# Optimization experiments

Hardware: AMD Instinct MI355X
Metric: run time of the kernel (lower is better)

Reference implementation:

```python
import jax, jax.numpy as jnp
import numpy as np

B, H, W = 32, 256, 256
K = 8          # nonzero voting centers per image
NPIX = 6       # corner pixels per center
MARGIN = 10.0
RATIO_INV = 1e4
LW = {'center': 1.0, 'corner': 1.0, 'corner_offset': 0.25, 'corner_bin_offset': 1.0}


def setup_inputs() -> dict:
    rng = np.random.default_rng(0)
    out0 = rng.standard_normal((B, 7, H, W)).astype(np.float32)
    out1 = rng.standard_normal((B, 7, H, W)).astype(np.float32)
    t_corner = np.zeros((B, 1, H, W), np.float32)
    t_corner_offset = np.zeros((B, 1, 2, H, W), np.float32)
    t_bin = rng.uniform(-0.5, 0.5, (B, 1, 2, H, W)).astype(np.float32)
    anchors = np.zeros((B, K + 1), np.int32)
    positives = np.zeros((B, K + 1), np.int32)
    neg_zero = np.zeros((B, K + 1), np.int32)
    neg_other = np.zeros((B, K), np.int32)
    for b in range(B):
        flat = rng.choice(H * W, size=K * NPIX, replace=False)
        ys, xs = flat // W, flat % W
        t_corner[b, 0, ys, xs] = 1.0
        cvals = rng.choice(np.arange(1, 1000), K, replace=False).astype(np.float32)
        for k in range(K):
            s = slice(k * NPIX, (k + 1) * NPIX)
            v = cvals[k] - (ys[s] + xs[s]).astype(np.float32)
            t_corner_offset[b, 0, 0, ys[s], xs[s]] = 0.5 * v
            t_corner_offset[b, 0, 1, ys[s], xs[s]] = 0.5 * v
        # reproduce the source's voting_map and its random triplet mining
        vm = t_corner_offset[b, 0, 0] + t_corner_offset[b, 0, 1]
        cy, cx = np.nonzero(t_corner[b, 0])
        vm = vm.copy()
        vm[cy, cx] += (cy + cx).astype(np.float32)
        vals = np.unique(vm)  # [0, c1..cK] sorted, zero first
        zero_flat = np.flatnonzero(vm.ravel() == 0)
        nz_flat = np.flatnonzero(vm.ravel() != 0)
        for ci, cv in enumerate(vals):
            idx = np.flatnonzero(vm.ravel() == cv)
            if cv == 0:
                a, p = rng.choice(idx, 2, replace=False)
                anchors[b, ci], positives[b, ci] = a, p
                neg_zero[b, ci] = rng.choice(nz_flat)
            else:
                if len(idx) > 1:
                    a, p = rng.choice(idx, 2, replace=False)
                else:
                    a = p = idx[0]
                anchors[b, ci], positives[b, ci] = a, p
                neg_zero[b, ci] = rng.choice(zero_flat)
                other = np.flatnonzero((vm.ravel() != 0) & (vm.ravel() != cv))
                neg_other[b, ci - 1] = rng.choice(other)
    return {
        'out0': jnp.asarray(out0), 'out1': jnp.asarray(out1),
        't_corner': jnp.asarray(t_corner),
        't_corner_offset': jnp.asarray(t_corner_offset),
        't_bin': jnp.asarray(t_bin),
        'anchors': jnp.asarray(anchors), 'positives': jnp.asarray(positives),
        'neg_zero': jnp.asarray(neg_zero), 'neg_other': jnp.asarray(neg_other),
    }


def _smooth_l1(d):
    ad = jnp.abs(d)
    return jnp.where(ad < 1.0, 0.5 * d * d, ad - 0.5)


def _losses_one_stack(output, t_corner, t_corner_offset, t_bin,
                      anchors, positives, neg_zero, neg_other):
    # output: [B,7,H,W] -> channel-major [7,B,H,W] (matches transpose(0,1).reshape)
    o = jnp.transpose(output, (1, 0, 2, 3))
    center = o[0]                                   # [B,H,W]  (n_jtyp=1)
    corner = o[1:3]                                 # [2,B,H,W]
    scale = jnp.array([H, W], jnp.float32)[:, None, None, None]
    corner_offset = jnp.tanh(o[3:5]) * scale        # [2,B,H,W]
    corner_bin = o[5:7]                             # [2,B,H,W]
    pos = t_corner[:, 0]                            # [B,H,W]

    # --- triplet loss on center predictions (pre-mined indices) ---
    pdf = center.reshape(B, -1)                     # [B,HW]
    va = jnp.take_along_axis(pdf, anchors, 1)       # [B,K+1]
    vp = jnp.take_along_axis(pdf, positives, 1)
    vn1 = jnp.take_along_axis(pdf, neg_zero, 1)
    vn2 = jnp.take_along_axis(pdf, neg_other, 1)    # [B,K]
    Dap = (va - vp) ** 2
    h1 = jax.nn.relu(Dap - (va - vn1) ** 2 + MARGIN)
    h2 = jax.nn.relu(Dap[:, 1:] - (va[:, 1:] - vn2) ** 2 + MARGIN)
    per_center = h1.at[:, 1:].set(0.5 * (h1[:, 1:] + h2))  # nonzero centers avg 2 hinges
    l_center = jnp.mean(jnp.sum(per_center, axis=1) / (K + 1))

    # --- corner cross entropy (ratio-weighted) ---
    nlogp = -jax.nn.log_softmax(corner, axis=0)     # [2,B,H,W]
    l_corner = jnp.mean(pos * nlogp[1] * RATIO_INV + (1.0 - pos) * nlogp[0], axis=(1, 2))

    # --- corner offset smooth-L1 heatmap loss, summed over the 2 coords ---
    tgt = jnp.transpose(t_corner_offset[:, 0], (1, 0, 2, 3))  # [2,B,H,W]
    mask = jnp.where(tgt != 0, RATIO_INV, 1.0)
    l_co = jnp.sum(jnp.mean(mask * _smooth_l1(corner_offset - tgt), axis=(2, 3)), axis=0)

    # --- corner bin offset sigmoid L1 with corner mask, summed over 2 coords ---
    tb = jnp.transpose(t_bin[:, 0], (1, 0, 2, 3))   # [2,B,H,W]
    w = jnp.mean(pos, axis=(1, 2), keepdims=True)   # [B,1,1]
    w = jnp.where(w == 0, 1.0, w)
    lb = jnp.abs(jax.nn.sigmoid(corner_bin) - 0.5 - tb) * (pos / w)[None]
    l_bo = jnp.sum(jnp.mean(lb, axis=(2, 3)), axis=0)

    return jnp.concatenate([
        jnp.array([l_center * LW['center']]),
        l_corner * LW['corner'],
        l_co * LW['corner_offset'],
        l_bo * LW['corner_bin_offset'],
    ])  # [1 + 3B]


def reference(out0, out1, t_corner, t_corner_offset, t_bin,
              anchors, positives, neg_zero, neg_other):
    s0 = _losses_one_stack(out0, t_corner, t_corner_offset, t_bin,
                           anchors, positives, neg_zero, neg_other)
    s1 = _losses_one_stack(out1, t_corner, t_corner_offset, t_bin,
                           anchors, positives, neg_zero, neg_other)
    return jnp.stack([s0, s1])  # [2, 1+3B]
```

## Files before the change

### kernel.cpp

```cpp
#include <hip/hip_runtime.h>

#define BB 32
#define HH 256
#define WW 256
#define HW (HH*WW)
#define HW4 (HW/4)
#define KP1 9
#define KNEG 8
#define MARGIN_F 10.0f
#define RATIO_INV_F 10000.0f

#define SLOT(i) ((i)*16)
#define WS_BYTES (226*16*4)

#define NSCAN 512
#define NGATH 4
#define NCE   1024
#define NCO   1024
#define GRID  (NSCAN + NGATH + NCE + NCO)

__device__ __forceinline__ float fast_tanh(float x) {
    float xc = fminf(fmaxf(x, -15.f), 15.f);
    float t = __expf(2.f * xc);
    return (t - 1.f) / (t + 1.f);
}
__device__ __forceinline__ float fast_sigmoid(float x) {
    return 1.f / (1.f + __expf(-x));
}
__device__ __forceinline__ float smooth_l1(float d) {
    float ad = fabsf(d);
    return ad < 1.f ? 0.5f * d * d : ad - 0.5f;
}
__device__ __forceinline__ float el(const float4& v, int j) {
    return reinterpret_cast<const float*>(&v)[j];
}
__device__ __forceinline__ float nlse0(float c0, float c1) {
    const float mx = fmaxf(c0, c1);
    return mx + __logf(1.f + __expf(-fabsf(c0 - c1))) - c0;
}
__device__ __forceinline__ void block_reduce_atomic(float x, float* dst,
                                                    float* scratch) {
    const int lane = threadIdx.x & 63;
    const int wid  = threadIdx.x >> 6;
#pragma unroll
    for (int off = 32; off; off >>= 1) x += __shfl_down(x, off);
    __syncthreads();
    if (lane == 0) scratch[wid] = x;
    __syncthreads();
    if (threadIdx.x == 0)
        atomicAdd(dst, scratch[0] + scratch[1] + scratch[2] + scratch[3]);
}

__global__ __launch_bounds__(256) void ml_fused_kernel(
    const float* __restrict__ out0, const float* __restrict__ out1,
    const float* __restrict__ t_corner, const float* __restrict__ t_co,
    const float* __restrict__ t_bin,
    const int* __restrict__ anchors, const int* __restrict__ positives,
    const int* __restrict__ neg_zero, const int* __restrict__ neg_other,
    float* __restrict__ acc)
{
    __shared__ float scratch[4];
    const int bid = blockIdx.x;
    const int t = threadIdx.x;

    if (bid < NSCAN) {
        const int b = bid >> 4;
        const int base = (bid & 15) * 1024;
        const float4* tc4 = (const float4*)(t_corner + (size_t)b * HW);
        float4 v[4];
#pragma unroll
        for (int k = 0; k < 4; ++k) v[k] = tc4[base + k * 256 + t];
        float s_pos = 0.f;
#pragma unroll
        for (int k = 0; k < 4; ++k) {
#pragma unroll
            for (int j = 0; j < 4; ++j) {
                const float pv = el(v[k], j);
                if (pv != 0.f) {
                    s_pos += pv;
                    const int p = 4 * (base + k * 256 + t) + j;
                    const float* oa = out0 + (size_t)b * 7 * HW;
                    const float* ob = out1 + (size_t)b * 7 * HW;
                    const float tb0 = t_bin[(size_t)b * 2 * HW + p];
                    const float tb1 = t_bin[(size_t)b * 2 * HW + HW + p];
                    const float a_c0 = oa[HW + p],    a_c1 = oa[2 * HW + p];
                    const float a_o5 = oa[5 * HW + p], a_o6 = oa[6 * HW + p];
                    const float b_c0 = ob[HW + p],    b_c1 = ob[2 * HW + p];
                    const float b_o5 = ob[5 * HW + p], b_o6 = ob[6 * HW + p];
                    {
                        const float mx = fmaxf(a_c0, a_c1);
                        const float lse = mx + __logf(1.f + __expf(-fabsf(a_c0 - a_c1)));
                        const float corr = pv * ((lse - a_c1) * RATIO_INV_F - (lse - a_c0));
                        atomicAdd(&acc[SLOT(32 + b)], corr);
                        const float sb0 = fabsf(fast_sigmoid(a_o5) - 0.5f - tb0);
                        const float sb1 = fabsf(fast_sigmoid(a_o6) - 0.5f - tb1);
                        atomicAdd(&acc[SLOT(160 + b)], (sb0 + sb1) * pv);
                    }
                    {
                        const float mx = fmaxf(b_c0, b_c1);
                        const float lse = mx + __logf(1.f + __expf(-fabsf(b_c0 - b_c1)));
                        const float corr = pv * ((lse - b_c1) * RATIO_INV_F - (lse - b_c0));
                        atomicAdd(&acc[SLOT(32 + 32 + b)], corr);
                        const float sb0 = fabsf(fast_sigmoid(b_o5) - 0.5f - tb0);
                        const float sb1 = fabsf(fast_sigmoid(b_o6) - 0.5f - tb1);
                        atomicAdd(&acc[SLOT(160 + 32 + b)], (sb0 + sb1) * pv);
                    }
                }
            }
        }
        block_reduce_atomic(s_pos, &acc[SLOT(b)], scratch);

    } else if (bid < NSCAN + NGATH) {
        const int gid = (bid - NSCAN) * 256 + t;
        float local0 = 0.f, local1 = 0.f;
        if (gid < 2 * BB * KP1) {
            const int s = gid / (BB * KP1);
            const int r = gid % (BB * KP1);
            const int b = r / KP1, c = r % KP1;
            const float* o = (s ? out1 : out0) + (size_t)b * 7 * HW;
            const int ia  = anchors  [b * KP1 + c];
            const int ip  = positives[b * KP1 + c];
            const int in1 = neg_zero [b * KP1 + c];
            const float va = o[ia], vp = o[ip], vn1 = o[in1];
            const float Dap = (va - vp) * (va - vp);
            const float h1 = fmaxf(0.f, Dap - (va - vn1) * (va - vn1) + MARGIN_F);
            float pc;
            if (c > 0) {
                const int in2 = neg_other[b * KNEG + (c - 1)];
                const float vn2 = o[in2];
                const float h2 = fmaxf(0.f, Dap - (va - vn2) * (va - vn2) + MARGIN_F);
                pc = 0.5f * (h1 + h2);
            } else {
                pc = h1;
            }
            if (s == 0) local0 = pc; else local1 = pc;
        }
        block_reduce_atomic(local0, &acc[SLOT(224)], scratch);
        block_reduce_atomic(local1, &acc[SLOT(225)], scratch);

    } else if (bid < NSCAN + NGATH + NCE) {
        const int r = bid - NSCAN - NGATH;
        const int img = r >> 4;
        const int s = img >> 5, b = img & 31;
        const int base = (r & 15) * 1024;
        const float* o = (s ? out1 : out0) + (size_t)b * 7 * HW;
        const float4* c1p = (const float4*)(o + HW);
        const float4* c2p = (const float4*)(o + 2 * HW);
        float4 v1[4], v2[4];
#pragma unroll
        for (int k = 0; k < 4; ++k) v1[k] = c1p[base + k * 256 + t];
#pragma unroll
        for (int k = 0; k < 4; ++k) v2[k] = c2p[base + k * 256 + t];
        float sum = 0.f;
#pragma unroll
        for (int k = 0; k < 4; ++k)
#pragma unroll
            for (int j = 0; j < 4; ++j)
                sum += nlse0(el(v1[k], j), el(v2[k], j));
        block_reduce_atomic(sum, &acc[SLOT(32 + s * 32 + b)], scratch);

    } else {
        const int r = bid - NSCAN - NGATH - NCE;
        const int b = r >> 5;
        const int base = (r & 31) * 512;
        const int p0 = base + t, p1 = base + 256 + t;
        const float4* tco4 = (const float4*)(t_co + (size_t)b * 2 * HW);
        const float4* o04  = (const float4*)(out0 + (size_t)b * 7 * HW);
        const float4* o14  = (const float4*)(out1 + (size_t)b * 7 * HW);
        const float4 tg0a = tco4[p0],           tg0b = tco4[p1];
        const float4 tg1a = tco4[HW4 + p0],     tg1b = tco4[HW4 + p1];
        const float4 a03a = o04[3 * HW4 + p0],  a03b = o04[3 * HW4 + p1];
        const float4 a04a = o04[4 * HW4 + p0],  a04b = o04[4 * HW4 + p1];
        const float4 a13a = o14[3 * HW4 + p0],  a13b = o14[3 * HW4 + p1];
        const float4 a14a = o14[4 * HW4 + p0],  a14b = o14[4 * HW4 + p1];
        float s0 = 0.f, s1 = 0.f;
#pragma unroll
        for (int j = 0; j < 4; ++j) {
            float tgt0 = el(tg0a, j), tgt1 = el(tg1a, j);
            float m0 = (tgt0 != 0.f) ? RATIO_INV_F : 1.f;
            float m1 = (tgt1 != 0.f) ? RATIO_INV_F : 1.f;
            s0 += m0 * smooth_l1(fast_tanh(el(a03a, j)) * (float)HH - tgt0)
                + m1 * smooth_l1(fast_tanh(el(a04a, j)) * (float)WW - tgt1);
            s1 += m0 * smooth_l1(fast_tanh(el(a13a, j)) * (float)HH - tgt0)
                + m1 * smooth_l1(fast_tanh(el(a14a, j)) * (float)WW - tgt1);
            tgt0 = el(tg0b, j); tgt1 = el(tg1b, j);
            m0 = (tgt0 != 0.f) ? RATIO_INV_F : 1.f;
            m1 = (tgt1 != 0.f) ? RATIO_INV_F : 1.f;
            s0 += m0 * smooth_l1(fast_tanh(el(a03b, j)) * (float)HH - tgt0)
                + m1 * smooth_l1(fast_tanh(el(a04b, j)) * (float)WW - tgt1);
            s1 += m0 * smooth_l1(fast_tanh(el(a13b, j)) * (float)HH - tgt0)
                + m1 * smooth_l1(fast_tanh(el(a14b, j)) * (float)WW - tgt1);
        }
        block_reduce_atomic(s0, &acc[SLOT(96 + b)], scratch);
        block_reduce_atomic(s1, &acc[SLOT(96 + 32 + b)], scratch);
    }
}

__global__ __launch_bounds__(256) void ml_finish_kernel(
    const float* __restrict__ acc, float* __restrict__ out)
{
    const int i = threadIdx.x;
    if (i >= 2 * 97) return;
    const int s = i / 97, j = i % 97;
    const float invHW = 1.f / (float)HW;
    float val;
    if (j == 0) {
        val = acc[SLOT(224 + s)] / (float)(KP1 * BB);
    } else if (j < 33) {
        const int b = j - 1;
        val = acc[SLOT(32 + s * 32 + b)] * invHW;
    } else if (j < 65) {
        const int b = j - 33;
        val = 0.25f * acc[SLOT(96 + s * 32 + b)] * invHW;
    } else {
        const int b = j - 65;
        const float sp = acc[SLOT(b)];
        val = (sp > 0.f) ? (acc[SLOT(160 + s * 32 + b)] / sp)
                         : (acc[SLOT(160 + s * 32 + b)] * invHW);
    }
    out[i] = val;
}

extern "C" void kernel_launch(void* const* d_in, const int* in_sizes, int n_in,
                              void* d_out, int out_size, void* d_ws, size_t ws_size,
                              hipStream_t stream) {
    const float* out0      = (const float*)d_in[0];
    const float* out1      = (const float*)d_in[1];
    const float* t_corner  = (const float*)d_in[2];
    const float* t_co      = (const float*)d_in[3];
    const float* t_bin     = (const float*)d_in[4];
    const int*   anchors   = (const int*)d_in[5];
    const int*   positives = (const int*)d_in[6];
    const int*   neg_zero  = (const int*)d_in[7];
    const int*   neg_other = (const int*)d_in[8];
    float* acc = (float*)d_ws;
    float* out = (float*)d_out;

    hipMemsetAsync(d_ws, 0, WS_BYTES, stream);

    ml_fused_kernel<<<GRID, 256, 0, stream>>>(out0, out1, t_corner, t_co, t_bin,
                                              anchors, positives, neg_zero,
                                              neg_other, acc);
    ml_finish_kernel<<<1, 256, 0, stream>>>(acc, out);
}
```

Before: 169.0 us.

## Fuse corner scan into CE blocks and replace atomics with per-block partial slots

The separate corner-mask scan blocks are merged into the stack-0 cross-entropy blocks, so each t_corner tile is read alongside the class channels it needs, and the scan block range goes away. Global atomicAdds and the workspace memset are replaced by per-block partial sums written to distinct slots, which the single-block finish kernel then reduces. This removes a memset launch, the atomic contention and one pass over t_corner. The cost is more serial work in the finish kernel and more block reductions per CE0 block.

```diff
diff --git a/kernel.cpp b/kernel.cpp
--- a/kernel.cpp
+++ b/kernel.cpp
@@ -10,14 +10,16 @@
 #define MARGIN_F 10.0f
 #define RATIO_INV_F 10000.0f
 
-#define SLOT(i) ((i)*16)
-#define WS_BYTES (226*16*4)
-
-#define NSCAN 512
 #define NGATH 4
-#define NCE   1024
 #define NCO   1024
-#define GRID  (NSCAN + NGATH + NCE + NCO)
+#define NCE0  512
+#define NCE1  512
+#define GATH_BASE 0
+#define CO_BASE   (NGATH)
+#define CE0_BASE  (NGATH + NCO)
+#define CE1_BASE  (NGATH + NCO + NCE0)
+#define GRID      (NGATH + NCO + NCE0 + NCE1)
+
 
 __device__ __forceinline__ float fast_tanh(float x) {
     float xc = fminf(fmaxf(x, -15.f), 15.f);
@@ -38,8 +40,7 @@
     const float mx = fmaxf(c0, c1);
     return mx + __logf(1.f + __expf(-fabsf(c0 - c1))) - c0;
 }
-__device__ __forceinline__ void block_reduce_atomic(float x, float* dst,
-                                                    float* scratch) {
+__device__ __forceinline__ float block_sum(float x, float* scratch) {
     const int lane = threadIdx.x & 63;
     const int wid  = threadIdx.x >> 6;
 #pragma unroll
@@ -47,71 +48,24 @@
     __syncthreads();
     if (lane == 0) scratch[wid] = x;
     __syncthreads();
-    if (threadIdx.x == 0)
-        atomicAdd(dst, scratch[0] + scratch[1] + scratch[2] + scratch[3]);
-}
-
-__global__ __launch_bounds__(256) void ml_fused_kernel(
+    return scratch[0] + scratch[1] + scratch[2] + scratch[3];
+}
+
+__global__ __launch_bounds__(256) void ml_partial_kernel(
     const float* __restrict__ out0, const float* __restrict__ out1,
     const float* __restrict__ t_corner, const float* __restrict__ t_co,
     const float* __restrict__ t_bin,
     const int* __restrict__ anchors, const int* __restrict__ positives,
     const int* __restrict__ neg_zero, const int* __restrict__ neg_other,
-    float* __restrict__ acc)
+    float* __restrict__ ws)
 {
     __shared__ float scratch[4];
     const int bid = blockIdx.x;
     const int t = threadIdx.x;
-
-    if (bid < NSCAN) {
-        const int b = bid >> 4;
-        const int base = (bid & 15) * 1024;
-        const float4* tc4 = (const float4*)(t_corner + (size_t)b * HW);
-        float4 v[4];
-#pragma unroll
-        for (int k = 0; k < 4; ++k) v[k] = tc4[base + k * 256 + t];
-        float s_pos = 0.f;
-#pragma unroll
-        for (int k = 0; k < 4; ++k) {
-#pragma unroll
-            for (int j = 0; j < 4; ++j) {
-                const float pv = el(v[k], j);
-                if (pv != 0.f) {
-                    s_pos += pv;
-                    const int p = 4 * (base + k * 256 + t) + j;
-                    const float* oa = out0 + (size_t)b * 7 * HW;
-                    const float* ob = out1 + (size_t)b * 7 * HW;
-                    const float tb0 = t_bin[(size_t)b * 2 * HW + p];
-                    const float tb1 = t_bin[(size_t)b * 2 * HW + HW + p];
-                    const float a_c0 = oa[HW + p],    a_c1 = oa[2 * HW + p];
-                    const float a_o5 = oa[5 * HW + p], a_o6 = oa[6 * HW + p];
-                    const float b_c0 = ob[HW + p],    b_c1 = ob[2 * HW + p];
-                    const float b_o5 = ob[5 * HW + p], b_o6 = ob[6 * HW + p];
-                    {
-                        const float mx = fmaxf(a_c0, a_c1);
-                        const float lse = mx + __logf(1.f + __expf(-fabsf(a_c0 - a_c1)));
-                        const float corr = pv * ((lse - a_c1) * RATIO_INV_F - (lse - a_c0));
-                        atomicAdd(&acc[SLOT(32 + b)], corr);
-                        const float sb0 = fabsf(fast_sigmoid(a_o5) - 0.5f - tb0);
-                        const float sb1 = fabsf(fast_sigmoid(a_o6) - 0.5f - tb1);
-                        atomicAdd(&acc[SLOT(160 + b)], (sb0 + sb1) * pv);
-                    }
-                    {
-                        const float mx = fmaxf(b_c0, b_c1);
-                        const float lse = mx + __logf(1.f + __expf(-fabsf(b_c0 - b_c1)));
-                        const float corr = pv * ((lse - b_c1) * RATIO_INV_F - (lse - b_c0));
-                        atomicAdd(&acc[SLOT(32 + 32 + b)], corr);
-                        const float sb0 = fabsf(fast_sigmoid(b_o5) - 0.5f - tb0);
-                        const float sb1 = fabsf(fast_sigmoid(b_o6) - 0.5f - tb1);
-                        atomicAdd(&acc[SLOT(160 + 32 + b)], (sb0 + sb1) * pv);
-                    }
-                }
-            }
-        }
-        block_reduce_atomic(s_pos, &acc[SLOT(b)], scratch);
-
-    } else if (bid < NSCAN + NGATH) {
-        const int gid = (bid - NSCAN) * 256 + t;
+    float* slot = ws + (size_t)bid * 8;
+
+    if (bid < NGATH) {
+        const int gid = bid * 256 + t;
         float local0 = 0.f, local1 = 0.f;
         if (gid < 2 * BB * KP1) {
             const int s = gid / (BB * KP1);
@@ -135,32 +89,12 @@
             }
             if (s == 0) local0 = pc; else local1 = pc;
         }
-        block_reduce_atomic(local0, &acc[SLOT(224)], scratch);
-        block_reduce_atomic(local1, &acc[SLOT(225)], scratch);
-
-    } else if (bid < NSCAN + NGATH + NCE) {
-        const int r = bid - NSCAN - NGATH;
-        const int img = r >> 4;
-        const int s = img >> 5, b = img & 31;
-        const int base = (r & 15) * 1024;
-        const float* o = (s ? out1 : out0) + (size_t)b * 7 * HW;
-        const float4* c1p = (const float4*)(o + HW);
-        const float4* c2p = (const float4*)(o + 2 * HW);
-        float4 v1[4], v2[4];
-#pragma unroll
-        for (int k = 0; k < 4; ++k) v1[k] = c1p[base + k * 256 + t];
-#pragma unroll
-        for (int k = 0; k < 4; ++k) v2[k] = c2p[base + k * 256 + t];
-        float sum = 0.f;
-#pragma unroll
-        for (int k = 0; k < 4; ++k)
-#pragma unroll
-            for (int j = 0; j < 4; ++j)
-                sum += nlse0(el(v1[k], j), el(v2[k], j));
-        block_reduce_atomic(sum, &acc[SLOT(32 + s * 32 + b)], scratch);
-
-    } else {
-        const int r = bid - NSCAN - NGATH - NCE;
+        const float r0 = block_sum(local0, scratch);
+        const float r1 = block_sum(local1, scratch);
+        if (t == 0) { slot[0] = r0; slot[1] = r1; }
+
+    } else if (bid < CE0_BASE) {
+        const int r = bid - CO_BASE;
         const int b = r >> 5;
         const int base = (r & 31) * 512;
         const int p0 = base + t, p1 = base + 256 + t;
@@ -191,13 +125,94 @@
             s1 += m0 * smooth_l1(fast_tanh(el(a13b, j)) * (float)HH - tgt0)
                 + m1 * smooth_l1(fast_tanh(el(a14b, j)) * (float)WW - tgt1);
         }
-        block_reduce_atomic(s0, &acc[SLOT(96 + b)], scratch);
-        block_reduce_atomic(s1, &acc[SLOT(96 + 32 + b)], scratch);
+        const float r0 = block_sum(s0, scratch);
+        const float r1 = block_sum(s1, scratch);
+        if (t == 0) { slot[0] = r0; slot[1] = r1; }
+
+    } else if (bid < CE1_BASE) {
+        const int r = bid - CE0_BASE;
+        const int b = r >> 4;
+        const int base = (r & 15) * 1024;
+        const float* oa = out0 + (size_t)b * 7 * HW;
+        const float* ob = out1 + (size_t)b * 7 * HW;
+        const float4* tc4 = (const float4*)(t_corner + (size_t)b * HW);
+        const float4* c1p = (const float4*)(oa + HW);
+        const float4* c2p = (const float4*)(oa + 2 * HW);
+        float4 tcv[4], v1[4], v2[4];
+#pragma unroll
+        for (int k = 0; k < 4; ++k) tcv[k] = tc4[base + k * 256 + t];
+#pragma unroll
+        for (int k = 0; k < 4; ++k) v1[k] = c1p[base + k * 256 + t];
+#pragma unroll
+        for (int k = 0; k < 4; ++k) v2[k] = c2p[base + k * 256 + t];
+
+        float ce0 = 0.f, s_pos = 0.f, corr1 = 0.f, bo0 = 0.f, bo1 = 0.f;
+#pragma unroll
+        for (int k = 0; k < 4; ++k) {
+#pragma unroll
+            for (int j = 0; j < 4; ++j) {
+                const float a_c0 = el(v1[k], j), a_c1 = el(v2[k], j);
+                ce0 += nlse0(a_c0, a_c1);
+                const float pv = el(tcv[k], j);
+                if (pv != 0.f) {
+                    s_pos += pv;
+                    const int p = 4 * (base + k * 256 + t) + j;
+                    const float tb0  = t_bin[(size_t)b * 2 * HW + p];
+                    const float tb1  = t_bin[(size_t)b * 2 * HW + HW + p];
+                    const float b_c0 = ob[HW + p],     b_c1 = ob[2 * HW + p];
+                    const float a_o5 = oa[5 * HW + p], a_o6 = oa[6 * HW + p];
+                    const float b_o5 = ob[5 * HW + p], b_o6 = ob[6 * HW + p];
+                    {
+                        const float mx = fmaxf(a_c0, a_c1);
+                        const float lse = mx + __logf(1.f + __expf(-fabsf(a_c0 - a_c1)));
+                        ce0 += pv * ((lse - a_c1) * RATIO_INV_F - (lse - a_c0));
+                        const float sb0 = fabsf(fast_sigmoid(a_o5) - 0.5f - tb0);
+                        const float sb1 = fabsf(fast_sigmoid(a_o6) - 0.5f - tb1);
+                        bo0 += (sb0 + sb1) * pv;
+                    }
+                    {
+                        const float mx = fmaxf(b_c0, b_c1);
+                        const float lse = mx + __logf(1.f + __expf(-fabsf(b_c0 - b_c1)));
+                        corr1 += pv * ((lse - b_c1) * RATIO_INV_F - (lse - b_c0));
+                        const float sb0 = fabsf(fast_sigmoid(b_o5) - 0.5f - tb0);
+                        const float sb1 = fabsf(fast_sigmoid(b_o6) - 0.5f - tb1);
+                        bo1 += (sb0 + sb1) * pv;
+                    }
+                }
+            }
+        }
+        const float r0 = block_sum(ce0,   scratch);
+        const float r1 = block_sum(s_pos, scratch);
+        const float r2 = block_sum(corr1, scratch);
+        const float r3 = block_sum(bo0,   scratch);
+        const float r4 = block_sum(bo1,   scratch);
+        if (t == 0) { slot[0]=r0; slot[1]=r1; slot[2]=r2; slot[3]=r3; slot[4]=r4; }
+
+    } else {
+        const int r = bid - CE1_BASE;
+        const int b = r >> 4;
+        const int base = (r & 15) * 1024;
+        const float* o = out1 + (size_t)b * 7 * HW;
+        const float4* c1p = (const float4*)(o + HW);
+        const float4* c2p = (const float4*)(o + 2 * HW);
+        float4 v1[4], v2[4];
+#pragma unroll
+        for (int k = 0; k < 4; ++k) v1[k] = c1p[base + k * 256 + t];
+#pragma unroll
+        for (int k = 0; k < 4; ++k) v2[k] = c2p[base + k * 256 + t];
+        float sum = 0.f;
+#pragma unroll
+        for (int k = 0; k < 4; ++k)
+#pragma unroll
+            for (int j = 0; j < 4; ++j)
+                sum += nlse0(el(v1[k], j), el(v2[k], j));
+        const float r0 = block_sum(sum, scratch);
+        if (t == 0) slot[0] = r0;
     }
 }
 
 __global__ __launch_bounds__(256) void ml_finish_kernel(
-    const float* __restrict__ acc, float* __restrict__ out)
+    const float* __restrict__ ws, float* __restrict__ out)
 {
     const int i = threadIdx.x;
     if (i >= 2 * 97) return;
@@ -205,18 +220,36 @@
     const float invHW = 1.f / (float)HW;
     float val;
     if (j == 0) {
-        val = acc[SLOT(224 + s)] / (float)(KP1 * BB);
+        float acc = 0.f;
+        for (int g = 0; g < NGATH; ++g) acc += ws[(size_t)(GATH_BASE + g) * 8 + s];
+        val = acc / (float)(KP1 * BB);
     } else if (j < 33) {
         const int b = j - 1;
-        val = acc[SLOT(32 + s * 32 + b)] * invHW;
+        float acc = 0.f;
+        if (s == 0) {
+            for (int k = 0; k < 16; ++k)
+                acc += ws[(size_t)(CE0_BASE + b * 16 + k) * 8 + 0];
+        } else {
+            for (int k = 0; k < 16; ++k)
+                acc += ws[(size_t)(CE1_BASE + b * 16 + k) * 8 + 0]
+                     + ws[(size_t)(CE0_BASE + b * 16 + k) * 8 + 2];
+        }
+        val = acc * invHW;
     } else if (j < 65) {
         const int b = j - 33;
-        val = 0.25f * acc[SLOT(96 + s * 32 + b)] * invHW;
+        float acc = 0.f;
+        for (int k = 0; k < 32; ++k)
+            acc += ws[(size_t)(CO_BASE + b * 32 + k) * 8 + s];
+        val = 0.25f * acc * invHW;
     } else {
         const int b = j - 65;
-        const float sp = acc[SLOT(b)];
-        val = (sp > 0.f) ? (acc[SLOT(160 + s * 32 + b)] / sp)
-                         : (acc[SLOT(160 + s * 32 + b)] * invHW);
+        float sp = 0.f, num = 0.f;
+        for (int k = 0; k < 16; ++k) {
+            const float* sl = ws + (size_t)(CE0_BASE + b * 16 + k) * 8;
+            sp  += sl[1];
+            num += sl[3 + s];
+        }
+        val = (sp > 0.f) ? (num / sp) : (num * invHW);
     }
     out[i] = val;
 }
@@ -233,13 +266,11 @@
     const int*   positives = (const int*)d_in[6];
     const int*   neg_zero  = (const int*)d_in[7];
     const int*   neg_other = (const int*)d_in[8];
-    float* acc = (float*)d_ws;
+    float* ws  = (float*)d_ws;
     float* out = (float*)d_out;
 
-    hipMemsetAsync(d_ws, 0, WS_BYTES, stream);
-
-    ml_fused_kernel<<<GRID, 256, 0, stream>>>(out0, out1, t_corner, t_co, t_bin,
-                                              anchors, positives, neg_zero,
-                                              neg_other, acc);
-    ml_finish_kernel<<<1, 256, 0, stream>>>(acc, out);
-}
+    ml_partial_kernel<<<GRID, 256, 0, stream>>>(out0, out1, t_corner, t_co, t_bin,
+                                                anchors, positives, neg_zero,
+                                                neg_other, ws);
+    ml_finish_kernel<<<1, 256, 0, stream>>>(ws, out);
+}
```

New measurement: 169.5 us. About the same (+0.3%).
